# Performance work log

Measured on AMD Instinct MI355X. Metric: run time of the kernel, lower is better.

The kernel has to match this reference:

```python
import jax, jax.numpy as jnp
import numpy as np

IN, OUT, IO, CF, CS = 128, 128, 512, 512, 1024
B = 8192
TAU_IO, TAU_CF, TAU_CS = 2.0, 5.0, 70.0


def _lin(x, W, b):
    # torch nn.Linear: y = x @ W.T + b, W has shape [out, in]
    return x @ W.T + b


def setup_inputs() -> dict:
    key = jax.random.key(0)
    ks = jax.random.split(key, 24)

    def wb(i, fan_out, fan_in):
        s = 1.0 / np.sqrt(fan_in)
        W = jax.random.uniform(ks[2 * i], (fan_out, fan_in), jnp.float32, -s, s)
        b = jax.random.uniform(ks[2 * i + 1], (fan_out,), jnp.float32, -s, s)
        return W, b

    Wi2io, bi2io = wb(0, IO, IN)
    Wio2o, bio2o = wb(1, OUT, IO)
    Wio2io, bio2io = wb(2, IO, IO)
    Wio2cf, bio2cf = wb(3, CF, IO)
    Wcf2io, bcf2io = wb(4, IO, CF)
    Wcf2cs, bcf2cs = wb(5, CS, CF)
    Wcf2cf, bcf2cf = wb(6, CF, CF)
    Wcs2cf, bcs2cf = wb(7, CF, CS)
    Wcs2cs, bcs2cs = wb(8, CS, CS)

    x = jax.random.normal(ks[18], (B, IN), jnp.float32)
    io_state = jnp.zeros((B, IO), jnp.float32)
    cf_state = jnp.zeros((B, CF), jnp.float32)
    cs_state = jnp.zeros((B, CS), jnp.float32)

    return dict(
        x=x, io_state=io_state, cf_state=cf_state, cs_state=cs_state,
        Wi2io=Wi2io, bi2io=bi2io, Wio2o=Wio2o, bio2o=bio2o,
        Wio2io=Wio2io, bio2io=bio2io, Wio2cf=Wio2cf, bio2cf=bio2cf,
        Wcf2io=Wcf2io, bcf2io=bcf2io, Wcf2cs=Wcf2cs, bcf2cs=bcf2cs,
        Wcf2cf=Wcf2cf, bcf2cf=bcf2cf, Wcs2cf=Wcs2cf, bcs2cf=bcs2cf,
        Wcs2cs=Wcs2cs, bcs2cs=bcs2cs,
    )


def reference(x, io_state, cf_state, cs_state,
              Wi2io, bi2io, Wio2o, bio2o,
              Wio2io, bio2io, Wio2cf, bio2cf,
              Wcf2io, bcf2io, Wcf2cs, bcf2cs,
              Wcf2cf, bcf2cf, Wcs2cf, bcs2cf,
              Wcs2cs, bcs2cs):
    x = x.reshape(-1, IN)
    # leaky-integrated updates; all branches read the *previous* states
    io_new = jnp.tanh(
        (1.0 - 1.0 / TAU_IO) * io_state
        + (_lin(io_state, Wio2io, bio2io)
           + _lin(cf_state, Wcf2io, bcf2io)
           + _lin(x, Wi2io, bi2io)) / TAU_IO)
    cf_new = jnp.tanh(
        (1.0 - 1.0 / TAU_CF) * cf_state
        + (_lin(cf_state, Wcf2cf, bcf2cf)
           + _lin(cs_state, Wcs2cf, bcs2cf)
           + _lin(io_state, Wio2cf, bio2cf)) / TAU_CF)
    cs_new = jnp.tanh(
        (1.0 - 1.0 / TAU_CS) * cs_state
        + (_lin(cs_state, Wcs2cs, bcs2cs)
           + _lin(cf_state, Wcf2cs, bcf2cs)) / TAU_CS)
    y = jnp.tanh(_lin(io_new, Wio2o, bio2o))
    return y
```

## Files before the change

kernel.cpp:

```cpp
#include <hip/hip_runtime.h>


typedef float f32x4 __attribute__((ext_vector_type(4)));
typedef __bf16 bf16x4 __attribute__((ext_vector_type(4)));
typedef __bf16 bf16x8 __attribute__((ext_vector_type(8)));
typedef unsigned short u16x4 __attribute__((ext_vector_type(4)));

__device__ __forceinline__ unsigned short f2bf(float f) {
    unsigned u = __builtin_bit_cast(unsigned, f);
    u += 0x7FFFu + ((u >> 16) & 1u);
    return (unsigned short)(u >> 16);
}

__device__ __forceinline__ float tanh_fast(float x) {
    float e = __expf(2.0f * x);
    return 1.0f - 2.0f * __builtin_amdgcn_rcpf(e + 1.0f);
}

__device__ __forceinline__ void gload16(const void* g, void* l) {
    __builtin_amdgcn_global_load_lds(
        (const __attribute__((address_space(1))) void*)g,
        (__attribute__((address_space(3))) void*)l, 16, 0, 0);
}

#define WAITB(N) asm volatile("s_waitcnt vmcnt(" #N ")\n\ts_barrier" ::: "memory")

__global__ __launch_bounds__(256) void k_convert(
    const float* __restrict__ Wi2io, const float* __restrict__ Wio2io,
    const float* __restrict__ Wcf2io, const float* __restrict__ Wio2o,
    const float* __restrict__ b1, const float* __restrict__ b2,
    const float* __restrict__ b3,
    unsigned short* __restrict__ wcat, unsigned short* __restrict__ w2s,
    float* __restrict__ bsum)
{
    int idx = blockIdx.x * 256 + threadIdx.x;
    if (idx < 147456) {
        int n = idx / 288;
        int k = (idx - n * 288) * 4;
        const float* s;
        if (k < 128)      s = Wi2io  + n * 128 + k;
        else if (k < 640) s = Wio2io + n * 512 + (k - 128);
        else              s = Wcf2io + n * 512 + (k - 640);
        f32x4 v = *(const f32x4*)s;
        u16x4 h;
        #pragma unroll
        for (int t = 0; t < 4; ++t) {
            float f = 0.5f * v[t];
            int kk = k + t;
            if (kk >= 128 && kk < 640 && (kk - 128) == n) f += 0.5f;
            h[t] = f2bf(f);
        }
        int ad = n * 1152 + (k & ~63) + ((((k >> 3) & 7) ^ (n & 7)) << 3) + (k & 7);
        *(u16x4*)(wcat + ad) = h;
    } else if (idx < 163840) {
        int q = idx - 147456;
        int n = q >> 7;
        int k = (q & 127) * 4;
        f32x4 v = *(const f32x4*)(Wio2o + n * 512 + k);
        u16x4 h; h[0]=f2bf(v[0]); h[1]=f2bf(v[1]); h[2]=f2bf(v[2]); h[3]=f2bf(v[3]);
        int ad = n * 512 + (k & ~63) + ((((k >> 3) & 7) ^ (n & 7)) << 3) + (k & 7);
        *(u16x4*)(w2s + ad) = h;
    } else if (idx < 164352) {
        int n = idx - 163840;
        bsum[n] = 0.5f * (b1[n] + b2[n] + b3[n]);
    }
}

__global__ __launch_bounds__(512, 2) void k_gemm1(
    const float* __restrict__ x, const float* __restrict__ io,
    const float* __restrict__ cf,
    const unsigned short* __restrict__ wcat,
    const float* __restrict__ bsum,
    unsigned short* __restrict__ ionew)
{
    __shared__ __align__(16) char lds[3][49152];

    const int tid = threadIdx.x, b = blockIdx.x;
    const int xcd = b & 7, idx = b >> 3;
    const int m0 = ((xcd << 3) | (idx & 7)) << 7;
    const int n0 = (idx >> 3) << 7;

    const int lane = tid & 63, wid = tid >> 6;
    const int li = lane & 15, lh = lane >> 4;
    const int wm = (wid >> 1) << 5;
    const int wn = (wid & 1) << 6;

    int a_off_x[4], a_off_s[4], b_off[2];
    #pragma unroll
    for (int j = 0; j < 4; ++j) {
        int r = (wid << 4) + (j << 2) + (lane >> 4);
        int cs = ((lane & 15) ^ (r & 15)) << 2;
        a_off_x[j] = (m0 + r) * 128 + cs;
        a_off_s[j] = (m0 + r) * 512 + cs;
    }
    #pragma unroll
    for (int j = 0; j < 2; ++j) {
        int rb = ((wid << 1) + j) * 8 + (lane >> 3);
        b_off[j] = (n0 + rb) * 1152 + ((lane & 7) << 3);
    }
    const int adstA = wid << 12;
    const int adstB = wid << 11;

    f32x4 zz = {0.f, 0.f, 0.f, 0.f};
    f32x4 acc[2][4];
    #pragma unroll
    for (int i = 0; i < 2; ++i)
        #pragma unroll
        for (int j = 0; j < 4; ++j) acc[i][j] = zz;

#define STAGE1(KT, BUF) do {                                                   \
        int K_ = (KT);                                                         \
        char* A_ = (BUF); char* B_ = (BUF) + 32768;                            \
        if (K_ < 2) {                                                          \
            const float* sp = x + (K_ << 6);                                   \
            _Pragma("unroll")                                                  \
            for (int j = 0; j < 4; ++j)                                        \
                gload16(sp + a_off_x[j], A_ + adstA + (j << 10));              \
        } else if (K_ < 10) {                                                  \
            const float* sp = io + ((K_ - 2) << 6);                            \
            _Pragma("unroll")                                                  \
            for (int j = 0; j < 4; ++j)                                        \
                gload16(sp + a_off_s[j], A_ + adstA + (j << 10));              \
        } else {                                                               \
            const float* sp = cf + ((K_ - 10) << 6);                           \
            _Pragma("unroll")                                                  \
            for (int j = 0; j < 4; ++j)                                        \
                gload16(sp + a_off_s[j], A_ + adstA + (j << 10));              \
        }                                                                      \
        const unsigned short* wp = wcat + (K_ << 6);                           \
        _Pragma("unroll")                                                      \
        for (int j = 0; j < 2; ++j)                                            \
            gload16(wp + b_off[j], B_ + adstB + (j << 10));                    \
    } while (0)

#define COMPUTE1(BUF) do {                                                     \
        const char* A_ = (BUF); const char* B_ = (BUF) + 32768;                \
        _Pragma("unroll")                                                      \
        for (int ks = 0; ks < 2; ++ks) {                                       \
            bf16x8 af[2];                                                      \
            _Pragma("unroll")                                                  \
            for (int mi = 0; mi < 2; ++mi) {                                   \
                int r = wm + mi * 16 + li;                                     \
                int c0 = ks * 8 + lh * 2;                                      \
                f32x4 a0 = *(const f32x4*)(A_ + r * 256 +                      \
                                           ((c0 ^ (r & 15)) << 4));            \
                f32x4 a1 = *(const f32x4*)(A_ + r * 256 +                      \
                                           (((c0 + 1) ^ (r & 15)) << 4));      \
                bf16x4 h0 = __builtin_convertvector(a0, bf16x4);               \
                bf16x4 h1 = __builtin_convertvector(a1, bf16x4);               \
                af[mi] = __builtin_shufflevector(h0, h1, 0,1,2,3,4,5,6,7);     \
            }                                                                  \
            _Pragma("unroll")                                                  \
            for (int nj = 0; nj < 4; ++nj) {                                   \
                int rb = wn + nj * 16 + li;                                    \
                int cb = ks * 4 + lh;                                          \
                bf16x8 bv = *(const bf16x8*)(B_ + rb * 128 +                   \
                                             ((cb ^ (rb & 7)) << 4));          \
                acc[0][nj] = __builtin_amdgcn_mfma_f32_16x16x32_bf16(          \
                    af[0], bv, acc[0][nj], 0, 0, 0);                           \
                acc[1][nj] = __builtin_amdgcn_mfma_f32_16x16x32_bf16(          \
                    af[1], bv, acc[1][nj], 0, 0, 0);                           \
            }                                                                  \
        }                                                                      \
    } while (0)

    STAGE1(0, lds[0]);
    STAGE1(1, lds[1]);
    char* p0 = lds[0]; char* p1 = lds[1]; char* p2 = lds[2];
    #pragma unroll 1
    for (int t = 0; t < 17; ++t) {
        WAITB(6);
        if (t + 2 < 18) STAGE1(t + 2, p2);
        COMPUTE1(p0);
        char* tmp = p0; p0 = p1; p1 = p2; p2 = tmp;
    }
    WAITB(0);
    COMPUTE1(p0);
#undef STAGE1
#undef COMPUTE1

    #pragma unroll
    for (int nj = 0; nj < 4; ++nj) {
        int gn = n0 + wn + nj * 16 + li;
        float bb = bsum[gn];
        #pragma unroll
        for (int mi = 0; mi < 2; ++mi) {
            #pragma unroll
            for (int r = 0; r < 4; ++r) {
                int gm = m0 + wm + mi * 16 + (lh << 2) + r;
                float v = tanh_fast(acc[mi][nj][r] + bb);
                int ad = gm * 512 + (gn & ~63) +
                         ((((gn >> 3) & 7) ^ (gm & 7)) << 3) + (gn & 7);
                ionew[ad] = f2bf(v);
            }
        }
    }
}

__global__ __launch_bounds__(256, 2) void k_gemm2(
    const unsigned short* __restrict__ ionew,
    const unsigned short* __restrict__ w2s,
    const float* __restrict__ b4,
    float* __restrict__ out)
{
    __shared__ __align__(16) char lds[3][20480];

    const int tid = threadIdx.x, b = blockIdx.x;
    const int xcd = b & 7, idx = b >> 3;
    const int m0 = ((xcd << 5) | idx) << 5;

    const int lane = tid & 63, wid = tid >> 6;
    const int li = lane & 15, lh = lane >> 4;
    const int wn = wid << 5;

    const int a2_off = (m0 + (wid << 3) + (lane >> 3)) * 512 + ((lane & 7) << 3);
    int b2_off[4];
    #pragma unroll
    for (int j = 0; j < 4; ++j)
        b2_off[j] = ((wid << 5) + 8 * j + (lane >> 3)) * 512 + ((lane & 7) << 3);

    f32x4 zz = {0.f, 0.f, 0.f, 0.f};
    f32x4 acc[2][2];
    acc[0][0] = zz; acc[0][1] = zz; acc[1][0] = zz; acc[1][1] = zz;

#define STAGE2(KT, BUF) do {                                                   \
        int K_ = (KT);                                                         \
        char* A_ = (BUF); char* B_ = (BUF) + 4096;                             \
        gload16(ionew + a2_off + (K_ << 6), A_ + (wid << 10));                 \
        _Pragma("unroll")                                                      \
        for (int j = 0; j < 4; ++j)                                            \
            gload16(w2s + b2_off[j] + (K_ << 6), B_ + (wid << 12) + j * 1024); \
    } while (0)

#define COMPUTE2(BUF) do {                                                     \
        const char* A_ = (BUF); const char* B_ = (BUF) + 4096;                 \
        _Pragma("unroll")                                                      \
        for (int ks = 0; ks < 2; ++ks) {                                       \
            int c = ks * 4 + lh;                                               \
            bf16x8 av[2];                                                      \
            _Pragma("unroll")                                                  \
            for (int mi = 0; mi < 2; ++mi) {                                   \
                int r = mi * 16 + li;                                          \
                av[mi] = *(const bf16x8*)(A_ + r * 128 + ((c ^ (r & 7)) << 4));\
            }                                                                  \
            _Pragma("unroll")                                                  \
            for (int nj = 0; nj < 2; ++nj) {                                   \
                int rb = wn + nj * 16 + li;                                    \
                bf16x8 bv = *(const bf16x8*)(B_ + rb * 128 +                   \
                                             ((c ^ (rb & 7)) << 4));           \
                acc[0][nj] = __builtin_amdgcn_mfma_f32_16x16x32_bf16(          \
                    av[0], bv, acc[0][nj], 0, 0, 0);                           \
                acc[1][nj] = __builtin_amdgcn_mfma_f32_16x16x32_bf16(          \
                    av[1], bv, acc[1][nj], 0, 0, 0);                           \
            }                                                                  \
        }                                                                      \
    } while (0)

    STAGE2(0, lds[0]);
    STAGE2(1, lds[1]);
    char* p0 = lds[0]; char* p1 = lds[1]; char* p2 = lds[2];
    #pragma unroll 1
    for (int t = 0; t < 7; ++t) {
        WAITB(5);
        if (t + 2 < 8) STAGE2(t + 2, p2);
        COMPUTE2(p0);
        char* tmp = p0; p0 = p1; p1 = p2; p2 = tmp;
    }
    WAITB(0);
    COMPUTE2(p0);
#undef STAGE2
#undef COMPUTE2

    #pragma unroll
    for (int nj = 0; nj < 2; ++nj) {
        int n = wn + nj * 16 + li;
        float bb = b4[n];
        #pragma unroll
        for (int mi = 0; mi < 2; ++mi) {
            #pragma unroll
            for (int r = 0; r < 4; ++r) {
                int gm = m0 + mi * 16 + (lh << 2) + r;
                out[(size_t)gm * 128 + n] = tanh_fast(acc[mi][nj][r] + bb);
            }
        }
    }
}

extern "C" void kernel_launch(void* const* d_in, const int* in_sizes, int n_in,
                              void* d_out, int out_size, void* d_ws, size_t ws_size,
                              hipStream_t stream)
{
    const float* x      = (const float*)d_in[0];
    const float* io     = (const float*)d_in[1];
    const float* cf     = (const float*)d_in[2];
    const float* Wi2io  = (const float*)d_in[4];
    const float* bi2io  = (const float*)d_in[5];
    const float* Wio2o  = (const float*)d_in[6];
    const float* bio2o  = (const float*)d_in[7];
    const float* Wio2io = (const float*)d_in[8];
    const float* bio2io = (const float*)d_in[9];
    const float* Wcf2io = (const float*)d_in[12];
    const float* bcf2io = (const float*)d_in[13];
    float* out = (float*)d_out;

    char* ws = (char*)d_ws;
    unsigned short* wcat  = (unsigned short*)ws;
    unsigned short* w2s   = (unsigned short*)(ws + 1179648);
    float*          bsum  = (float*)(ws + 1310720);
    unsigned short* ionew = (unsigned short*)(ws + 1312768);

    hipLaunchKernelGGL(k_convert, dim3(642), dim3(256), 0, stream,
                       Wi2io, Wio2io, Wcf2io, Wio2o, bi2io, bio2io, bcf2io,
                       wcat, w2s, bsum);
    hipLaunchKernelGGL(k_gemm1, dim3(256), dim3(512), 0, stream,
                       x, io, cf, wcat, bsum, ionew);
    hipLaunchKernelGGL(k_gemm2, dim3(256), dim3(256), 0, stream,
                       ionew, w2s, bio2o, out);
}
```

Baseline: 32.88 us.

## Stage activations through registers and convert to bf16 before LDS write

The A-operand path of the first GEMM now loads fp32 activations into registers, converts them to bf16 and writes them to LDS, replacing direct global-to-LDS fp32 copies. This halves the A-tile LDS footprint (48KB to 32KB per stage) and removes repeated fp32-to-bf16 conversion and the doubled LDS reads inside the MFMA loop. The pipeline is restructured into a two-step unrolled loop with register double-buffering and an lgkmcnt wait in the barrier. The cost is more VGPR pressure and explicit vector-load latency exposure in the main loop.

```diff
diff --git a/kernel.cpp b/kernel.cpp
--- a/kernel.cpp
+++ b/kernel.cpp
@@ -23,7 +23,7 @@
         (__attribute__((address_space(3))) void*)l, 16, 0, 0);
 }
 
-#define WAITB(N) asm volatile("s_waitcnt vmcnt(" #N ")\n\ts_barrier" ::: "memory")
+#define WAITB(N) asm volatile("s_waitcnt vmcnt(" #N ") lgkmcnt(0)\n\ts_barrier" ::: "memory")
 
 __global__ __launch_bounds__(256) void k_convert(
     const float* __restrict__ Wi2io, const float* __restrict__ Wio2io,
@@ -73,7 +73,7 @@
     const float* __restrict__ bsum,
     unsigned short* __restrict__ ionew)
 {
-    __shared__ __align__(16) char lds[3][49152];
+    __shared__ __align__(16) char lds[3][32768];
 
     const int tid = threadIdx.x, b = blockIdx.x;
     const int xcd = b & 7, idx = b >> 3;
@@ -85,22 +85,21 @@
     const int wm = (wid >> 1) << 5;
     const int wn = (wid & 1) << 6;
 
-    int a_off_x[4], a_off_s[4], b_off[2];
-    #pragma unroll
-    for (int j = 0; j < 4; ++j) {
-        int r = (wid << 4) + (j << 2) + (lane >> 4);
-        int cs = ((lane & 15) ^ (r & 15)) << 2;
-        a_off_x[j] = (m0 + r) * 128 + cs;
-        a_off_s[j] = (m0 + r) * 512 + cs;
-    }
+    const int row0 = tid >> 3, ch = tid & 7;
+    const size_t aoffx0 = (size_t)(m0 + row0) * 128 + ch * 8;
+    const size_t aoffx1 = (size_t)(m0 + row0 + 64) * 128 + ch * 8;
+    const size_t aoffs0 = (size_t)(m0 + row0) * 512 + ch * 8;
+    const size_t aoffs1 = (size_t)(m0 + row0 + 64) * 512 + ch * 8;
+    const int lwa0 = row0 * 128 + ((ch ^ (row0 & 7)) << 4);
+    int b_off[2];
     #pragma unroll
     for (int j = 0; j < 2; ++j) {
         int rb = ((wid << 1) + j) * 8 + (lane >> 3);
         b_off[j] = (n0 + rb) * 1152 + ((lane & 7) << 3);
     }
-    const int adstA = wid << 12;
     const int adstB = wid << 11;
 
+    f32x4 qa0, qa1, qa2, qa3, ra0, ra1, ra2, ra3;
     f32x4 zz = {0.f, 0.f, 0.f, 0.f};
     f32x4 acc[2][4];
     #pragma unroll
@@ -108,54 +107,53 @@
         #pragma unroll
         for (int j = 0; j < 4; ++j) acc[i][j] = zz;
 
-#define STAGE1(KT, BUF) do {                                                   \
+#define ALOAD(S0, S1, S2, S3, KT) do {                                         \
         int K_ = (KT);                                                         \
-        char* A_ = (BUF); char* B_ = (BUF) + 32768;                            \
-        if (K_ < 2) {                                                          \
-            const float* sp = x + (K_ << 6);                                   \
-            _Pragma("unroll")                                                  \
-            for (int j = 0; j < 4; ++j)                                        \
-                gload16(sp + a_off_x[j], A_ + adstA + (j << 10));              \
-        } else if (K_ < 10) {                                                  \
-            const float* sp = io + ((K_ - 2) << 6);                            \
-            _Pragma("unroll")                                                  \
-            for (int j = 0; j < 4; ++j)                                        \
-                gload16(sp + a_off_s[j], A_ + adstA + (j << 10));              \
-        } else {                                                               \
-            const float* sp = cf + ((K_ - 10) << 6);                           \
-            _Pragma("unroll")                                                  \
-            for (int j = 0; j < 4; ++j)                                        \
-                gload16(sp + a_off_s[j], A_ + adstA + (j << 10));              \
-        }                                                                      \
-        const unsigned short* wp = wcat + (K_ << 6);                           \
-        _Pragma("unroll")                                                      \
-        for (int j = 0; j < 2; ++j)                                            \
-            gload16(wp + b_off[j], B_ + adstB + (j << 10));                    \
+        const float* sp; size_t o0, o1;                                        \
+        if (K_ < 2)       { sp = x  + (K_ << 6);        o0 = aoffx0; o1 = aoffx1; } \
+        else if (K_ < 10) { sp = io + ((K_ - 2) << 6);  o0 = aoffs0; o1 = aoffs1; } \
+        else              { sp = cf + ((K_ - 10) << 6); o0 = aoffs0; o1 = aoffs1; } \
+        S0 = *(const f32x4*)(sp + o0);                                         \
+        S1 = *(const f32x4*)(sp + o0 + 4);                                     \
+        S2 = *(const f32x4*)(sp + o1);                                         \
+        S3 = *(const f32x4*)(sp + o1 + 4);                                     \
+    } while (0)
+
+#define BSTAGE(KT, BUF) do {                                                   \
+        const unsigned short* wp = wcat + ((KT) << 6);                         \
+        char* B_ = (BUF) + 16384;                                              \
+        gload16(wp + b_off[0], B_ + adstB);                                    \
+        gload16(wp + b_off[1], B_ + adstB + 1024);                             \
+    } while (0)
+
+#define AWRITE(S0, S1, S2, S3, BUF) do {                                       \
+        char* A_ = (BUF);                                                      \
+        bf16x4 h0 = __builtin_convertvector(S0, bf16x4);                       \
+        bf16x4 h1 = __builtin_convertvector(S1, bf16x4);                       \
+        bf16x4 h2 = __builtin_convertvector(S2, bf16x4);                       \
+        bf16x4 h3 = __builtin_convertvector(S3, bf16x4);                       \
+        *(bf16x8*)(A_ + lwa0) =                                                \
+            __builtin_shufflevector(h0, h1, 0,1,2,3,4,5,6,7);                  \
+        *(bf16x8*)(A_ + lwa0 + 8192) =                                         \
+            __builtin_shufflevector(h2, h3, 0,1,2,3,4,5,6,7);                  \
     } while (0)
 
 #define COMPUTE1(BUF) do {                                                     \
-        const char* A_ = (BUF); const char* B_ = (BUF) + 32768;                \
+        const char* A_ = (BUF); const char* B_ = (BUF) + 16384;                \
         _Pragma("unroll")                                                      \
         for (int ks = 0; ks < 2; ++ks) {                                       \
+            int c = ks * 4 + lh;                                               \
             bf16x8 af[2];                                                      \
             _Pragma("unroll")                                                  \
             for (int mi = 0; mi < 2; ++mi) {                                   \
                 int r = wm + mi * 16 + li;                                     \
-                int c0 = ks * 8 + lh * 2;                                      \
-                f32x4 a0 = *(const f32x4*)(A_ + r * 256 +                      \
-                                           ((c0 ^ (r & 15)) << 4));            \
-                f32x4 a1 = *(const f32x4*)(A_ + r * 256 +                      \
-                                           (((c0 + 1) ^ (r & 15)) << 4));      \
-                bf16x4 h0 = __builtin_convertvector(a0, bf16x4);               \
-                bf16x4 h1 = __builtin_convertvector(a1, bf16x4);               \
-                af[mi] = __builtin_shufflevector(h0, h1, 0,1,2,3,4,5,6,7);     \
+                af[mi] = *(const bf16x8*)(A_ + r * 128 + ((c ^ (r & 7)) << 4));\
             }                                                                  \
             _Pragma("unroll")                                                  \
             for (int nj = 0; nj < 4; ++nj) {                                   \
                 int rb = wn + nj * 16 + li;                                    \
-                int cb = ks * 4 + lh;                                          \
                 bf16x8 bv = *(const bf16x8*)(B_ + rb * 128 +                   \
-                                             ((cb ^ (rb & 7)) << 4));          \
+                                             ((c ^ (rb & 7)) << 4));           \
                 acc[0][nj] = __builtin_amdgcn_mfma_f32_16x16x32_bf16(          \
                     af[0], bv, acc[0][nj], 0, 0, 0);                           \
                 acc[1][nj] = __builtin_amdgcn_mfma_f32_16x16x32_bf16(          \
@@ -164,20 +162,44 @@
         }                                                                      \
     } while (0)
 
-    STAGE1(0, lds[0]);
-    STAGE1(1, lds[1]);
     char* p0 = lds[0]; char* p1 = lds[1]; char* p2 = lds[2];
+#define ROT() do { char* t_ = p0; p0 = p1; p1 = p2; p2 = t_; } while (0)
+
+    ALOAD(qa0, qa1, qa2, qa3, 0);
+    BSTAGE(0, p0);
+    ALOAD(ra0, ra1, ra2, ra3, 1);
+    BSTAGE(1, p1);
+    asm volatile("s_waitcnt vmcnt(8)" ::: "memory");
+    AWRITE(qa0, qa1, qa2, qa3, p0);
+
     #pragma unroll 1
-    for (int t = 0; t < 17; ++t) {
-        WAITB(6);
-        if (t + 2 < 18) STAGE1(t + 2, p2);
+    for (int i = 0; i < 8; ++i) {
+        WAITB(2);
+        ALOAD(qa0, qa1, qa2, qa3, 2 * i + 2);
+        BSTAGE(2 * i + 2, p2);
+        AWRITE(ra0, ra1, ra2, ra3, p1);
         COMPUTE1(p0);
-        char* tmp = p0; p0 = p1; p1 = p2; p2 = tmp;
-    }
+        ROT();
+        WAITB(2);
+        if (2 * i + 3 < 18) {
+            ALOAD(ra0, ra1, ra2, ra3, 2 * i + 3);
+            BSTAGE(2 * i + 3, p2);
+        }
+        AWRITE(qa0, qa1, qa2, qa3, p1);
+        COMPUTE1(p0);
+        ROT();
+    }
+    WAITB(2);
+    AWRITE(ra0, ra1, ra2, ra3, p1);
+    COMPUTE1(p0);
+    ROT();
     WAITB(0);
     COMPUTE1(p0);
-#undef STAGE1
+#undef ALOAD
+#undef BSTAGE
+#undef AWRITE
 #undef COMPUTE1
+#undef ROT
 
     #pragma unroll
     for (int nj = 0; nj < 4; ++nj) {
```

New measurement: 37.87 us. +15.2%, slower.

## Load GEMM1 weights as pre-swizzled MFMA fragments directly into registers

Applied to the files above, without the earlier changes.

The weight conversion kernel now writes the concatenated bf16 weights in an MFMA fragment-major layout. GEMM1 can then load each B operand straight from global memory into registers instead of staging it through LDS. The GEMM1 tile shrinks to 64x128, the LDS buffers shrink to A-only 16 KB stages, and the grid doubles to 512 blocks at higher occupancy. This removes LDS traffic and bank pressure for B and improves wave occupancy, but weight loads now hit L2 directly with global latency exposed inside each iteration.

```diff
diff --git a/kernel.cpp b/kernel.cpp
--- a/kernel.cpp
+++ b/kernel.cpp
@@ -30,7 +30,7 @@
     const float* __restrict__ Wcf2io, const float* __restrict__ Wio2o,
     const float* __restrict__ b1, const float* __restrict__ b2,
     const float* __restrict__ b3,
-    unsigned short* __restrict__ wcat, unsigned short* __restrict__ w2s,
+    unsigned short* __restrict__ wfrag, unsigned short* __restrict__ w2s,
     float* __restrict__ bsum)
 {
     int idx = blockIdx.x * 256 + threadIdx.x;
@@ -50,8 +50,10 @@
             if (kk >= 128 && kk < 640 && (kk - 128) == n) f += 0.5f;
             h[t] = f2bf(f);
         }
-        int ad = n * 1152 + (k & ~63) + ((((k >> 3) & 7) ^ (n & 7)) << 3) + (k & 7);
-        *(u16x4*)(wcat + ad) = h;
+        int kt = k >> 6, ks = (k >> 5) & 1, c16 = n >> 4;
+        int l = (n & 15) | (((k >> 3) & 3) << 4);
+        int ad = ((((kt << 5) | c16) << 1) | ks) * 512 + l * 8 + (k & 7);
+        *(u16x4*)(wfrag + ad) = h;
     } else if (idx < 163840) {
         int q = idx - 147456;
         int n = q >> 7;
@@ -66,75 +68,70 @@
     }
 }
 
-__global__ __launch_bounds__(512, 2) void k_gemm1(
+__global__ __launch_bounds__(512, 4) void k_gemm1(
     const float* __restrict__ x, const float* __restrict__ io,
     const float* __restrict__ cf,
-    const unsigned short* __restrict__ wcat,
+    const unsigned short* __restrict__ wfrag,
     const float* __restrict__ bsum,
     unsigned short* __restrict__ ionew)
 {
-    __shared__ __align__(16) char lds[3][49152];
+    __shared__ __align__(16) char lds[3][16384];
 
     const int tid = threadIdx.x, b = blockIdx.x;
     const int xcd = b & 7, idx = b >> 3;
-    const int m0 = ((xcd << 3) | (idx & 7)) << 7;
-    const int n0 = (idx >> 3) << 7;
+    const int m0 = ((xcd << 4) | (idx & 15)) << 6;
+    const int n0 = (idx >> 4) << 7;
 
     const int lane = tid & 63, wid = tid >> 6;
     const int li = lane & 15, lh = lane >> 4;
-    const int wm = (wid >> 1) << 5;
-    const int wn = (wid & 1) << 6;
-
-    int a_off_x[4], a_off_s[4], b_off[2];
-    #pragma unroll
-    for (int j = 0; j < 4; ++j) {
-        int r = (wid << 4) + (j << 2) + (lane >> 4);
-        int cs = ((lane & 15) ^ (r & 15)) << 2;
-        a_off_x[j] = (m0 + r) * 128 + cs;
-        a_off_s[j] = (m0 + r) * 512 + cs;
-    }
+    const int wm = (wid >> 2) << 5;
+    const int wn = (wid & 3) << 5;
+
+    int a_off_x[2], a_off_s[2];
     #pragma unroll
     for (int j = 0; j < 2; ++j) {
-        int rb = ((wid << 1) + j) * 8 + (lane >> 3);
-        b_off[j] = (n0 + rb) * 1152 + ((lane & 7) << 3);
-    }
-    const int adstA = wid << 12;
-    const int adstB = wid << 11;
+        int rw = (wid << 3) + (j << 2) + (lane >> 4);
+        int cs = (lane & 15) ^ (rw & 15);
+        a_off_x[j] = (m0 + rw) * 128 + cs * 4;
+        a_off_s[j] = (m0 + rw) * 512 + cs * 4;
+    }
+    const int adst = wid << 11;
+
+    const unsigned short* fb = wfrag + (size_t)(((n0 + wn) >> 4)) * 1024 + lane * 8;
 
     f32x4 zz = {0.f, 0.f, 0.f, 0.f};
-    f32x4 acc[2][4];
-    #pragma unroll
-    for (int i = 0; i < 2; ++i)
-        #pragma unroll
-        for (int j = 0; j < 4; ++j) acc[i][j] = zz;
-
-#define STAGE1(KT, BUF) do {                                                   \
+    f32x4 acc[2][2];
+    acc[0][0] = zz; acc[0][1] = zz; acc[1][0] = zz; acc[1][1] = zz;
+    bf16x8 b00, b01, b10, b11;
+
+#define ASTAGE(KT, BUF) do {                                                   \
         int K_ = (KT);                                                         \
-        char* A_ = (BUF); char* B_ = (BUF) + 32768;                            \
+        char* A_ = (BUF);                                                      \
         if (K_ < 2) {                                                          \
             const float* sp = x + (K_ << 6);                                   \
-            _Pragma("unroll")                                                  \
-            for (int j = 0; j < 4; ++j)                                        \
-                gload16(sp + a_off_x[j], A_ + adstA + (j << 10));              \
+            gload16(sp + a_off_x[0], A_ + adst);                               \
+            gload16(sp + a_off_x[1], A_ + adst + 1024);                        \
         } else if (K_ < 10) {                                                  \
             const float* sp = io + ((K_ - 2) << 6);                            \
-            _Pragma("unroll")                                                  \
-            for (int j = 0; j < 4; ++j)                                        \
-                gload16(sp + a_off_s[j], A_ + adstA + (j << 10));              \
+            gload16(sp + a_off_s[0], A_ + adst);                               \
+            gload16(sp + a_off_s[1], A_ + adst + 1024);                        \
         } else {                                                               \
             const float* sp = cf + ((K_ - 10) << 6);                           \
-            _Pragma("unroll")                                                  \
-            for (int j = 0; j < 4; ++j)                                        \
-                gload16(sp + a_off_s[j], A_ + adstA + (j << 10));              \
+            gload16(sp + a_off_s[0], A_ + adst);                               \
+            gload16(sp + a_off_s[1], A_ + adst + 1024);                        \
         }                                                                      \
-        const unsigned short* wp = wcat + (K_ << 6);                           \
-        _Pragma("unroll")                                                      \
-        for (int j = 0; j < 2; ++j)                                            \
-            gload16(wp + b_off[j], B_ + adstB + (j << 10));                    \
+    } while (0)
+
+#define BLOAD(KT) do {                                                         \
+        const unsigned short* fp = fb + (size_t)(KT) * 32768;                  \
+        b00 = *(const bf16x8*)(fp);                                            \
+        b01 = *(const bf16x8*)(fp + 512);                                      \
+        b10 = *(const bf16x8*)(fp + 1024);                                     \
+        b11 = *(const bf16x8*)(fp + 1536);                                     \
     } while (0)
 
 #define COMPUTE1(BUF) do {                                                     \
-        const char* A_ = (BUF); const char* B_ = (BUF) + 32768;                \
+        const char* A_ = (BUF);                                                \
         _Pragma("unroll")                                                      \
         for (int ks = 0; ks < 2; ++ks) {                                       \
             bf16x8 af[2];                                                      \
@@ -150,37 +147,36 @@
                 bf16x4 h1 = __builtin_convertvector(a1, bf16x4);               \
                 af[mi] = __builtin_shufflevector(h0, h1, 0,1,2,3,4,5,6,7);     \
             }                                                                  \
-            _Pragma("unroll")                                                  \
-            for (int nj = 0; nj < 4; ++nj) {                                   \
-                int rb = wn + nj * 16 + li;                                    \
-                int cb = ks * 4 + lh;                                          \
-                bf16x8 bv = *(const bf16x8*)(B_ + rb * 128 +                   \
-                                             ((cb ^ (rb & 7)) << 4));          \
-                acc[0][nj] = __builtin_amdgcn_mfma_f32_16x16x32_bf16(          \
-                    af[0], bv, acc[0][nj], 0, 0, 0);                           \
-                acc[1][nj] = __builtin_amdgcn_mfma_f32_16x16x32_bf16(          \
-                    af[1], bv, acc[1][nj], 0, 0, 0);                           \
-            }                                                                  \
+            bf16x8 bv0 = ks ? b01 : b00;                                       \
+            bf16x8 bv1 = ks ? b11 : b10;                                       \
+            acc[0][0] = __builtin_amdgcn_mfma_f32_16x16x32_bf16(               \
+                af[0], bv0, acc[0][0], 0, 0, 0);                               \
+            acc[1][0] = __builtin_amdgcn_mfma_f32_16x16x32_bf16(               \
+                af[1], bv0, acc[1][0], 0, 0, 0);                               \
+            acc[0][1] = __builtin_amdgcn_mfma_f32_16x16x32_bf16(               \
+                af[0], bv1, acc[0][1], 0, 0, 0);                               \
+            acc[1][1] = __builtin_amdgcn_mfma_f32_16x16x32_bf16(               \
+                af[1], bv1, acc[1][1], 0, 0, 0);                               \
         }                                                                      \
     } while (0)
 
-    STAGE1(0, lds[0]);
-    STAGE1(1, lds[1]);
+    ASTAGE(0, lds[0]);
+    ASTAGE(1, lds[1]);
     char* p0 = lds[0]; char* p1 = lds[1]; char* p2 = lds[2];
     #pragma unroll 1
-    for (int t = 0; t < 17; ++t) {
-        WAITB(6);
-        if (t + 2 < 18) STAGE1(t + 2, p2);
+    for (int t = 0; t < 18; ++t) {
+        if (t < 17) { WAITB(2); } else { WAITB(0); }
+        BLOAD(t);
+        if (t + 2 < 18) ASTAGE(t + 2, p2);
         COMPUTE1(p0);
         char* tmp = p0; p0 = p1; p1 = p2; p2 = tmp;
     }
-    WAITB(0);
-    COMPUTE1(p0);
-#undef STAGE1
+#undef ASTAGE
+#undef BLOAD
 #undef COMPUTE1
 
     #pragma unroll
-    for (int nj = 0; nj < 4; ++nj) {
+    for (int nj = 0; nj < 2; ++nj) {
         int gn = n0 + wn + nj * 16 + li;
         float bb = bsum[gn];
         #pragma unroll
@@ -304,16 +300,16 @@
     float* out = (float*)d_out;
 
     char* ws = (char*)d_ws;
-    unsigned short* wcat  = (unsigned short*)ws;
+    unsigned short* wfrag = (unsigned short*)ws;
     unsigned short* w2s   = (unsigned short*)(ws + 1179648);
     float*          bsum  = (float*)(ws + 1310720);
     unsigned short* ionew = (unsigned short*)(ws + 1312768);
 
     hipLaunchKernelGGL(k_convert, dim3(642), dim3(256), 0, stream,
                        Wi2io, Wio2io, Wcf2io, Wio2o, bi2io, bio2io, bcf2io,
-                       wcat, w2s, bsum);
-    hipLaunchKernelGGL(k_gemm1, dim3(256), dim3(512), 0, stream,
-                       x, io, cf, wcat, bsum, ionew);
+                       wfrag, w2s, bsum);
+    hipLaunchKernelGGL(k_gemm1, dim3(512), dim3(512), 0, stream,
+                       x, io, cf, wfrag, bsum, ionew);
     hipLaunchKernelGGL(k_gemm2, dim3(256), dim3(256), 0, stream,
                        ionew, w2s, bio2o, out);
 }
```

New measurement: 35.19 us. 7.0% more time.

## Pre-convert activations to swizzled bf16 in prep kernel before GEMM1

Applied to the files above, without the earlier changes.

Adds a prep pass that converts x, io_state and cf_state to one concatenated, swizzled bf16 matrix, and merges weight conversion into the same kernel. GEMM1 then loads bf16 A tiles directly, halving its A-tile LDS footprint and removing the in-loop fp32-to-bf16 conversion. The cost is an extra full write and read of the activation matrix through global memory.

```diff
diff --git a/kernel.cpp b/kernel.cpp
--- a/kernel.cpp
+++ b/kernel.cpp
@@ -25,55 +25,78 @@
 
 #define WAITB(N) asm volatile("s_waitcnt vmcnt(" #N ")\n\ts_barrier" ::: "memory")
 
-__global__ __launch_bounds__(256) void k_convert(
+__device__ __forceinline__ int swz_ad(int row, int k, int L) {
+    return row * L + (k & ~63) + ((((k >> 3) & 7) ^ (row & 7)) << 3) + (k & 7);
+}
+
+__global__ __launch_bounds__(256) void k_prep(
+    const float* __restrict__ x, const float* __restrict__ io,
+    const float* __restrict__ cf,
     const float* __restrict__ Wi2io, const float* __restrict__ Wio2io,
     const float* __restrict__ Wcf2io, const float* __restrict__ Wio2o,
     const float* __restrict__ b1, const float* __restrict__ b2,
     const float* __restrict__ b3,
-    unsigned short* __restrict__ wcat, unsigned short* __restrict__ w2s,
-    float* __restrict__ bsum)
+    unsigned short* __restrict__ abf16, unsigned short* __restrict__ wcat,
+    unsigned short* __restrict__ w2s, float* __restrict__ bsum)
 {
     int idx = blockIdx.x * 256 + threadIdx.x;
-    if (idx < 147456) {
-        int n = idx / 288;
-        int k = (idx - n * 288) * 4;
+    if (idx < 1179648) {
+        int m = idx / 144;
+        int k = (idx - m * 144) * 8;
+        const float* s;
+        if (k < 128)      s = x  + m * 128 + k;
+        else if (k < 640) s = io + m * 512 + (k - 128);
+        else              s = cf + m * 512 + (k - 640);
+        f32x4 v0 = *(const f32x4*)s;
+        f32x4 v1 = *(const f32x4*)(s + 4);
+        bf16x4 h0 = __builtin_convertvector(v0, bf16x4);
+        bf16x4 h1 = __builtin_convertvector(v1, bf16x4);
+        *(bf16x8*)(abf16 + swz_ad(m, k, 1152)) =
+            __builtin_shufflevector(h0, h1, 0,1,2,3,4,5,6,7);
+    } else if (idx < 1253376) {
+        int q = idx - 1179648;
+        int n = q / 144;
+        int k = (q - n * 144) * 8;
         const float* s;
         if (k < 128)      s = Wi2io  + n * 128 + k;
         else if (k < 640) s = Wio2io + n * 512 + (k - 128);
         else              s = Wcf2io + n * 512 + (k - 640);
-        f32x4 v = *(const f32x4*)s;
-        u16x4 h;
-        #pragma unroll
-        for (int t = 0; t < 4; ++t) {
-            float f = 0.5f * v[t];
+        f32x4 v0 = *(const f32x4*)s;
+        f32x4 v1 = *(const f32x4*)(s + 4);
+        float w[8];
+        #pragma unroll
+        for (int t = 0; t < 4; ++t) { w[t] = 0.5f * v0[t]; w[t+4] = 0.5f * v1[t]; }
+        #pragma unroll
+        for (int t = 0; t < 8; ++t) {
             int kk = k + t;
-            if (kk >= 128 && kk < 640 && (kk - 128) == n) f += 0.5f;
-            h[t] = f2bf(f);
+            if (kk >= 128 && kk < 640 && (kk - 128) == n) w[t] += 0.5f;
         }
-        int ad = n * 1152 + (k & ~63) + ((((k >> 3) & 7) ^ (n & 7)) << 3) + (k & 7);
-        *(u16x4*)(wcat + ad) = h;
-    } else if (idx < 163840) {
-        int q = idx - 147456;
-        int n = q >> 7;
-        int k = (q & 127) * 4;
-        f32x4 v = *(const f32x4*)(Wio2o + n * 512 + k);
-        u16x4 h; h[0]=f2bf(v[0]); h[1]=f2bf(v[1]); h[2]=f2bf(v[2]); h[3]=f2bf(v[3]);
-        int ad = n * 512 + (k & ~63) + ((((k >> 3) & 7) ^ (n & 7)) << 3) + (k & 7);
-        *(u16x4*)(w2s + ad) = h;
-    } else if (idx < 164352) {
-        int n = idx - 163840;
+        unsigned short* dst = wcat + swz_ad(n, k, 1152);
+        #pragma unroll
+        for (int t = 0; t < 8; ++t) dst[t] = f2bf(w[t]);
+    } else if (idx < 1261568) {
+        int q = idx - 1253376;
+        int n = q >> 6;
+        int k = (q & 63) * 8;
+        f32x4 v0 = *(const f32x4*)(Wio2o + n * 512 + k);
+        f32x4 v1 = *(const f32x4*)(Wio2o + n * 512 + k + 4);
+        bf16x4 h0 = __builtin_convertvector(v0, bf16x4);
+        bf16x4 h1 = __builtin_convertvector(v1, bf16x4);
+        *(bf16x8*)(w2s + swz_ad(n, k, 512)) =
+            __builtin_shufflevector(h0, h1, 0,1,2,3,4,5,6,7);
+    } else if (idx < 1262080) {
+        int n = idx - 1261568;
         bsum[n] = 0.5f * (b1[n] + b2[n] + b3[n]);
     }
 }
 
 __global__ __launch_bounds__(512, 2) void k_gemm1(
-    const float* __restrict__ x, const float* __restrict__ io,
-    const float* __restrict__ cf,
+    const unsigned short* __restrict__ abf16,
     const unsigned short* __restrict__ wcat,
     const float* __restrict__ bsum,
     unsigned short* __restrict__ ionew)
 {
-    __shared__ __align__(16) char lds[3][49152];
+    __shared__ __align__(16) char lds[3][32768];
 
     const int tid = threadIdx.x, b = blockIdx.x;
     const int xcd = b & 7, idx = b >> 3;
@@ -85,21 +108,15 @@
     const int wm = (wid >> 1) << 5;
     const int wn = (wid & 1) << 6;
 
-    int a_off_x[4], a_off_s[4], b_off[2];
-    #pragma unroll
-    for (int j = 0; j < 4; ++j) {
-        int r = (wid << 4) + (j << 2) + (lane >> 4);
-        int cs = ((lane & 15) ^ (r & 15)) << 2;
-        a_off_x[j] = (m0 + r) * 128 + cs;
-        a_off_s[j] = (m0 + r) * 512 + cs;
-    }
+    int a_off[2], b_off[2];
     #pragma unroll
     for (int j = 0; j < 2; ++j) {
-        int rb = ((wid << 1) + j) * 8 + (lane >> 3);
+        int ra = (wid << 4) + (j << 3) + (lane >> 3);
+        a_off[j] = (m0 + ra) * 1152 + ((lane & 7) << 3);
+        int rb = (wid << 4) + (j << 3) + (lane >> 3);
         b_off[j] = (n0 + rb) * 1152 + ((lane & 7) << 3);
     }
-    const int adstA = wid << 12;
-    const int adstB = wid << 11;
+    const int adst = wid << 11;
 
     f32x4 zz = {0.f, 0.f, 0.f, 0.f};
     f32x4 acc[2][4];
@@ -110,52 +127,31 @@
 
 #define STAGE1(KT, BUF) do {                                                   \
         int K_ = (KT);                                                         \
-        char* A_ = (BUF); char* B_ = (BUF) + 32768;                            \
-        if (K_ < 2) {                                                          \
-            const float* sp = x + (K_ << 6);                                   \
-            _Pragma("unroll")                                                  \
-            for (int j = 0; j < 4; ++j)                                        \
-                gload16(sp + a_off_x[j], A_ + adstA + (j << 10));              \
-        } else if (K_ < 10) {                                                  \
-            const float* sp = io + ((K_ - 2) << 6);                            \
-            _Pragma("unroll")                                                  \
-            for (int j = 0; j < 4; ++j)                                        \
-                gload16(sp + a_off_s[j], A_ + adstA + (j << 10));              \
-        } else {                                                               \
-            const float* sp = cf + ((K_ - 10) << 6);                           \
-            _Pragma("unroll")                                                  \
-            for (int j = 0; j < 4; ++j)                                        \
-                gload16(sp + a_off_s[j], A_ + adstA + (j << 10));              \
-        }                                                                      \
+        char* A_ = (BUF); char* B_ = (BUF) + 16384;                            \
+        const unsigned short* ap = abf16 + (K_ << 6);                          \
+        gload16(ap + a_off[0], A_ + adst);                                     \
+        gload16(ap + a_off[1], A_ + adst + 1024);                              \
         const unsigned short* wp = wcat + (K_ << 6);                           \
-        _Pragma("unroll")                                                      \
-        for (int j = 0; j < 2; ++j)                                            \
-            gload16(wp + b_off[j], B_ + adstB + (j << 10));                    \
+        gload16(wp + b_off[0], B_ + adst);                                     \
+        gload16(wp + b_off[1], B_ + adst + 1024);                              \
     } while (0)
 
 #define COMPUTE1(BUF) do {                                                     \
-        const char* A_ = (BUF); const char* B_ = (BUF) + 32768;                \
+        const char* A_ = (BUF); const char* B_ = (BUF) + 16384;                \
         _Pragma("unroll")                                                      \
         for (int ks = 0; ks < 2; ++ks) {                                       \
+            int c = ks * 4 + lh;                                               \
             bf16x8 af[2];                                                      \
             _Pragma("unroll")                                                  \
             for (int mi = 0; mi < 2; ++mi) {                                   \
                 int r = wm + mi * 16 + li;                                     \
-                int c0 = ks * 8 + lh * 2;                                      \
-                f32x4 a0 = *(const f32x4*)(A_ + r * 256 +                      \
-                                           ((c0 ^ (r & 15)) << 4));            \
-                f32x4 a1 = *(const f32x4*)(A_ + r * 256 +                      \
-                                           (((c0 + 1) ^ (r & 15)) << 4));      \
-                bf16x4 h0 = __builtin_convertvector(a0, bf16x4);               \
-                bf16x4 h1 = __builtin_convertvector(a1, bf16x4);               \
-                af[mi] = __builtin_shufflevector(h0, h1, 0,1,2,3,4,5,6,7);     \
+                af[mi] = *(const bf16x8*)(A_ + r * 128 + ((c ^ (r & 7)) << 4));\
             }                                                                  \
             _Pragma("unroll")                                                  \
             for (int nj = 0; nj < 4; ++nj) {                                   \
                 int rb = wn + nj * 16 + li;                                    \
-                int cb = ks * 4 + lh;                                          \
                 bf16x8 bv = *(const bf16x8*)(B_ + rb * 128 +                   \
-                                             ((cb ^ (rb & 7)) << 4));          \
+                                             ((c ^ (rb & 7)) << 4));           \
                 acc[0][nj] = __builtin_amdgcn_mfma_f32_16x16x32_bf16(          \
                     af[0], bv, acc[0][nj], 0, 0, 0);                           \
                 acc[1][nj] = __builtin_amdgcn_mfma_f32_16x16x32_bf16(          \
@@ -168,14 +164,12 @@
     STAGE1(1, lds[1]);
     char* p0 = lds[0]; char* p1 = lds[1]; char* p2 = lds[2];
     #pragma unroll 1
-    for (int t = 0; t < 17; ++t) {
-        WAITB(6);
+    for (int t = 0; t < 18; ++t) {
+        if (t < 17) { WAITB(4); } else { WAITB(0); }
         if (t + 2 < 18) STAGE1(t + 2, p2);
         COMPUTE1(p0);
         char* tmp = p0; p0 = p1; p1 = p2; p2 = tmp;
     }
-    WAITB(0);
-    COMPUTE1(p0);
 #undef STAGE1
 #undef COMPUTE1
 
@@ -189,9 +183,7 @@
             for (int r = 0; r < 4; ++r) {
                 int gm = m0 + wm + mi * 16 + (lh << 2) + r;
                 float v = tanh_fast(acc[mi][nj][r] + bb);
-                int ad = gm * 512 + (gn & ~63) +
-                         ((((gn >> 3) & 7) ^ (gm & 7)) << 3) + (gn & 7);
-                ionew[ad] = f2bf(v);
+                ionew[swz_ad(gm, gn, 512)] = f2bf(v);
             }
         }
     }
@@ -304,16 +296,17 @@
     float* out = (float*)d_out;
 
     char* ws = (char*)d_ws;
-    unsigned short* wcat  = (unsigned short*)ws;
-    unsigned short* w2s   = (unsigned short*)(ws + 1179648);
-    float*          bsum  = (float*)(ws + 1310720);
-    unsigned short* ionew = (unsigned short*)(ws + 1312768);
-
-    hipLaunchKernelGGL(k_convert, dim3(642), dim3(256), 0, stream,
-                       Wi2io, Wio2io, Wcf2io, Wio2o, bi2io, bio2io, bcf2io,
-                       wcat, w2s, bsum);
+    unsigned short* abf16 = (unsigned short*)ws;
+    unsigned short* wcat  = (unsigned short*)(ws + 18874368);
+    unsigned short* w2s   = (unsigned short*)(ws + 20054016);
+    float*          bsum  = (float*)(ws + 20185088);
+    unsigned short* ionew = (unsigned short*)(ws + 20187136);
+
+    hipLaunchKernelGGL(k_prep, dim3(4930), dim3(256), 0, stream,
+                       x, io, cf, Wi2io, Wio2io, Wcf2io, Wio2o,
+                       bi2io, bio2io, bcf2io, abf16, wcat, w2s, bsum);
     hipLaunchKernelGGL(k_gemm1, dim3(256), dim3(512), 0, stream,
-                       x, io, cf, wcat, bsum, ionew);
+                       abf16, wcat, bsum, ionew);
     hipLaunchKernelGGL(k_gemm2, dim3(256), dim3(256), 0, stream,
                        ionew, w2s, bio2o, out);
 }
```

Result: no change. 33.47 us (+1.8%).
